# Optimization experiments

Hardware: AMD Instinct MI355X
Metric: run time of the kernel (lower is better)

The kernel has to match this reference:

```python
import jax, jax.numpy as jnp
import numpy as np

N_NODES = 100000
N_EDGES = 1600000
MIN_NORM = 1e-15
EPS_F32 = 4e-3  # PoincareBall eps for float32


def _norm(x):
    return jnp.clip(jnp.linalg.norm(x, axis=-1, keepdims=True), MIN_NORM)


def artanh(x):
    x = jnp.clip(x, -1.0 + 1e-15, 1.0 - 1e-15)
    return 0.5 * (jnp.log1p(x) - jnp.log1p(-x))


def proj(x, c):
    norm = _norm(x)
    maxnorm = (1.0 - EPS_F32) / jnp.sqrt(c)
    return jnp.where(norm > maxnorm, x / norm * maxnorm, x)


def expmap0(u, c):
    sqrt_c = jnp.sqrt(c)
    u_norm = _norm(u)
    return jnp.tanh(sqrt_c * u_norm) * u / (sqrt_c * u_norm)


def logmap0(p, c):
    sqrt_c = jnp.sqrt(c)
    p_norm = _norm(p)
    return artanh(sqrt_c * p_norm) * p / (sqrt_c * p_norm)


def mobius_add(x, y, c):
    x2 = jnp.sum(x * x, axis=-1, keepdims=True)
    y2 = jnp.sum(y * y, axis=-1, keepdims=True)
    xy = jnp.sum(x * y, axis=-1, keepdims=True)
    num = (1.0 + 2.0 * c * xy + c * y2) * x + (1.0 - c * x2) * y
    denom = 1.0 + 2.0 * c * xy + (c ** 2) * x2 * y2
    return num / jnp.clip(denom, MIN_NORM)


def mobius_matvec(m, x, c):
    sqrt_c = jnp.sqrt(c)
    x_norm = _norm(x)
    mx = x @ m.T  # [N, out]
    mx_norm = _norm(mx)
    res = jnp.tanh(mx_norm / x_norm * artanh(sqrt_c * x_norm)) * mx / (mx_norm * sqrt_c)
    cond = jnp.all(mx == 0.0, axis=-1, keepdims=True)
    return jnp.where(cond, 0.0, res)


def hyp_linear(x, w, b, c):
    mv = proj(mobius_matvec(w, x, c), c)
    hyp_bias = proj(expmap0(b[None, :], c), c)  # proj_tan0 is identity on Poincare ball
    return proj(mobius_add(mv, hyp_bias, c), c)


def hyp_agg(x, edge_row, edge_col, edge_weight, c):
    x_tan = logmap0(x, c)
    msgs = edge_weight[:, None] * x_tan[edge_col]  # gather source features
    support = jax.ops.segment_sum(msgs, edge_row, num_segments=N_NODES)
    return proj(expmap0(support, c), c)


def hyp_act(x, c_in, c_out):
    xt = jax.nn.relu(logmap0(x, c_in))  # proj_tan0 identity
    return proj(expmap0(xt, c_out), c_out)


def setup_inputs() -> dict:
    key = jax.random.key(0)
    ks = jax.random.split(key, 10)
    x = jax.random.normal(ks[0], (N_NODES, 1433), dtype=jnp.float32)
    edge_row = jax.random.randint(ks[1], (N_EDGES,), 0, N_NODES, dtype=jnp.int32)
    edge_col = jax.random.randint(ks[2], (N_EDGES,), 0, N_NODES, dtype=jnp.int32)
    edge_weight = jax.random.uniform(ks[3], (N_EDGES,), dtype=jnp.float32)
    w1 = jax.random.normal(ks[4], (100, 1433), dtype=jnp.float32) * 0.05
    b1 = jax.random.normal(ks[5], (100,), dtype=jnp.float32) * 0.05
    w2 = jax.random.normal(ks[6], (64, 100), dtype=jnp.float32) * 0.05
    b2 = jax.random.normal(ks[7], (64,), dtype=jnp.float32) * 0.05
    lin_w = jax.random.normal(ks[8], (7, 64), dtype=jnp.float32) * 0.05
    lin_b = jax.random.normal(ks[9], (7,), dtype=jnp.float32) * 0.05
    return {"x": x, "edge_row": edge_row, "edge_col": edge_col,
            "edge_weight": edge_weight, "w1": w1, "b1": b1,
            "w2": w2, "b2": b2, "lin_w": lin_w, "lin_b": lin_b}


def reference(x, edge_row, edge_col, edge_weight, w1, b1, w2, b2, lin_w, lin_b):
    c = 1.0
    # encode: tangent -> hyperbolic (proj_tan0 is identity)
    h = proj(expmap0(x, c), c)
    # layer 1: HypLinear -> HypAgg -> HypAct
    h = hyp_linear(h, w1, b1, c)
    h = hyp_agg(h, edge_row, edge_col, edge_weight, c)
    h = hyp_act(h, c, c)
    # layer 2
    h = hyp_linear(h, w2, b2, c)
    h = hyp_agg(h, edge_row, edge_col, edge_weight, c)
    h = hyp_act(h, c, c)
    # decode: logmap0 -> Linear(64,7) with relu -> log_softmax
    t = logmap0(h, c)
    logits = jax.nn.relu(t @ lin_w.T + lin_b)
    return jax.nn.log_softmax(logits, axis=-1)
```

## Files before the change

### kernel.cpp

```cpp
#include <hip/hip_runtime.h>
#include <hip/hip_bf16.h>
#include <math.h>

#define MINN 1e-15f
#define MAXN 0.996f

#define KPAD 1472

typedef __attribute__((ext_vector_type(8))) short short8;
typedef __attribute__((ext_vector_type(4))) float f32x4;

__device__ __forceinline__ float artanhf_(float v){
  v = fminf(fmaxf(v, -0.9999999f), 0.9999999f);
  return 0.5f*(log1pf(v) - log1pf(-v));
}
__device__ __forceinline__ float grp8(float v){
  v += __shfl_xor(v,1,8); v += __shfl_xor(v,2,8); v += __shfl_xor(v,4,8); return v;
}
__device__ __forceinline__ float grp16w(float v){
  v += __shfl_xor(v,1,16); v += __shfl_xor(v,2,16);
  v += __shfl_xor(v,4,16); v += __shfl_xor(v,8,16); return v;
}
__device__ __forceinline__ unsigned short f2bf(float f){
  unsigned int u = __float_as_uint(f);
  unsigned int r = (u + 0x7fffu + ((u >> 16) & 1u)) >> 16;
  return (unsigned short)r;
}
__device__ __forceinline__ float bf2f(unsigned short h){
  return __uint_as_float(((unsigned int)h) << 16);
}
__device__ __forceinline__ unsigned short f2bf_c(float f){
  __hip_bfloat16 b = __float2bfloat16(f);
  return *reinterpret_cast<unsigned short*>(&b);
}

typedef __attribute__((address_space(1))) const unsigned int gu32;
typedef __attribute__((address_space(3))) unsigned int su32;
__device__ __forceinline__ void gload_lds16(const void* g, void* s){
  __builtin_amdgcn_global_load_lds((gu32*)g, (su32*)s, 16, 0, 0);
}

__global__ __launch_bounds__(256) void k_prep_w1b16(const float* __restrict__ w1,
    unsigned short* __restrict__ w1hi, unsigned short* __restrict__ w1lo){
  int idx = blockIdx.x*256 + threadIdx.x;
  int col = idx / KPAD, k = idx - col*KPAD;
  float v = (col < 100 && k < 1433) ? w1[(size_t)col*1433 + k] : 0.f;
  unsigned short h = f2bf(v);
  unsigned short lo = f2bf(v - bf2f(h));
  w1hi[idx] = h; w1lo[idx] = lo;
}

__global__ void k_bias(const float* __restrict__ b1, const float* __restrict__ b2,
                       float* __restrict__ hb1, float* __restrict__ hb2, float* __restrict__ scal){
  __shared__ float red[128];
  int t = threadIdx.x;
  float v = (t < 100) ? b1[t] : 0.f;
  red[t] = v*v; __syncthreads();
  for (int s=64;s;s>>=1){ if (t<s) red[t]+=red[t+s]; __syncthreads(); }
  float n2 = red[0]; __syncthreads();
  float n = fmaxf(sqrtf(n2), MINN);
  float s1 = tanhf(n)/n;
  float pn = fmaxf(tanhf(n), MINN);
  float t1 = pn > MAXN ? MAXN/pn : 1.f;
  float hv = s1*t1*v;
  hb1[t] = (t<100) ? hv : 0.f;
  red[t] = (t<100) ? hv*hv : 0.f; __syncthreads();
  for (int s=64;s;s>>=1){ if (t<s) red[t]+=red[t+s]; __syncthreads(); }
  if (t==0) scal[0] = red[0];
  __syncthreads();
  float v2 = (t < 64) ? b2[t] : 0.f;
  red[t] = v2*v2; __syncthreads();
  for (int s=64;s;s>>=1){ if (t<s) red[t]+=red[t+s]; __syncthreads(); }
  float n2b = red[0]; __syncthreads();
  float nb = fmaxf(sqrtf(n2b), MINN);
  float s1b = tanhf(nb)/nb;
  float pnb = fmaxf(tanhf(nb), MINN);
  float t1b = pnb > MAXN ? MAXN/pnb : 1.f;
  float hvb = s1b*t1b*v2;
  if (t < 64) hb2[t] = hvb;
  red[t] = (t<64) ? hvb*hvb : 0.f; __syncthreads();
  for (int s=64;s;s>>=1){ if (t<s) red[t]+=red[t+s]; __syncthreads(); }
  if (t==0) scal[1] = red[0];
}

__global__ __launch_bounds__(512) void k_lin1_mfma(
    const float* __restrict__ x, const unsigned short* __restrict__ w1hi,
    const unsigned short* __restrict__ w1lo, const float* __restrict__ hb1,
    const float* __restrict__ scal, unsigned short* __restrict__ xtan1, int N)
{
  __shared__ alignas(16) char bsm[2*28*1024];
  int tid = threadIdx.x;
  int w = tid >> 6, l = tid & 63;
  int lr = l & 15, lg = l >> 4;
  int bm = blockIdx.x * 128;
  int row0 = bm + w*16;
  int r = row0 + lr;
  const float* xr = x + (size_t)min(r, N-1)*1433 + lg*8;
  float b1sq = scal[0];

  f32x4 acc[7];
  #pragma unroll
  for (int t=0;t<7;t++) acc[t] = (f32x4){0.f,0.f,0.f,0.f};
  float sq = 0.f;

  auto stage = [&](int buf, int kbase){
    #pragma unroll
    for (int c = 0; c < 4; ++c){
      int cc = w + 8*c;
      if (cc < 28){
        int h = (cc >= 14) ? 1 : 0;
        int rem = cc - h*14;
        int t = (rem < 7) ? rem : rem - 7;
        const unsigned short* arr = (rem < 7) ? w1hi : w1lo;
        const unsigned short* src = arr + (size_t)(t*16 + lr)*KPAD + kbase + h*32 + lg*8;
        gload_lds16(src, bsm + (buf*28 + cc)*1024);
      }
    }
  };
  auto xload = [&](float* d, int kbase){
    #pragma unroll
    for (int h = 0; h < 2; ++h){
      int kk = kbase + h*32;
      const float* p = xr + kk;
      if (kk + 32 <= 1433) {
        #pragma unroll
        for (int j=0;j<8;j++) d[h*8+j] = p[j];
      } else {
        #pragma unroll
        for (int j=0;j<8;j++){
          bool kv = (kk + lg*8 + j) < 1433;
          d[h*8+j] = kv ? p[j] : 0.f;
        }
      }
    }
  };

  stage(0, 0);
  float xa[16];
  xload(xa, 0);
  __syncthreads();

  for (int kb = 0; kb < 23; ++kb) {
    int cur = kb & 1, nxt = cur ^ 1;
    int nk = (kb + 1) * 64;

    float xb[16];
    if (kb + 1 < 23){
      stage(nxt, nk);
      xload(xb, nk);
    } else {
      #pragma unroll
      for (int j=0;j<16;j++) xb[j] = 0.f;
    }

    #pragma unroll
    for (int h = 0; h < 2; ++h){
      short8 ah, al;
      #pragma unroll
      for (int j=0;j<8;j++){
        float v = xa[h*8+j];
        sq = fmaf(v, v, sq);
        unsigned short hu = f2bf_c(v);
        ah[j] = (short)hu;
        float hf = bf2f(hu);
        al[j] = (short)f2bf_c(v - hf);
      }
      const char* base = bsm + (cur*28 + h*14)*1024 + (l << 4);
      short8 bh[7], bl[7];
      #pragma unroll
      for (int t=0;t<7;t++){
        bh[t] = *reinterpret_cast<const short8*>(base + t*1024);
        bl[t] = *reinterpret_cast<const short8*>(base + (7+t)*1024);
      }
      #pragma unroll
      for (int t=0;t<7;t++){
        acc[t] = __builtin_amdgcn_mfma_f32_16x16x32_bf16(ah, bh[t], acc[t], 0,0,0);
        acc[t] = __builtin_amdgcn_mfma_f32_16x16x32_bf16(al, bh[t], acc[t], 0,0,0);
        acc[t] = __builtin_amdgcn_mfma_f32_16x16x32_bf16(ah, bl[t], acc[t], 0,0,0);
      }
    }
    #pragma unroll
    for (int j=0;j<16;j++) xa[j] = xb[j];

    __syncthreads();
  }

  sq += __shfl_xor(sq, 16); sq += __shfl_xor(sq, 32);

  float hbv[7];
  #pragma unroll
  for (int t=0;t<7;t++) hbv[t] = hb1[t*16 + lr];

  #pragma unroll
  for (int r4=0;r4<4;r4++){
    int rrow = 4*lg + r4;
    float v[7];
    #pragma unroll
    for (int t=0;t<7;t++) v[t] = acc[t][r4];
    float yn2 = 0.f, dotb = 0.f;
    #pragma unroll
    for (int t=0;t<7;t++){ yn2 += v[t]*v[t]; dotb += v[t]*hbv[t]; }
    yn2 = grp16w(yn2); dotb = grp16w(dotb);
    float xn2 = __shfl(sq, rrow);

    float un = fmaxf(sqrtf(xn2), MINN);
    float th = tanhf(un);
    float sE = th/un;
    float pn = fmaxf(th, MINN);
    float t1 = pn > MAXN ? MAXN/pn : 1.f;
    float gam = sE*t1;
    float xh = fmaxf(gam*un, MINN);
    float yn = sqrtf(yn2);
    float mxn = fmaxf(gam*yn, MINN);
    float rs = tanhf(mxn/xh*artanhf_(xh))/mxn;
    if (yn2 == 0.f) rs = 0.f;
    float rn = rs*gam*yn;
    float t2 = rn > MAXN ? MAXN/fmaxf(rn,MINN) : 1.f;
    float alpha = t2*rs*gam;
    float x2v = alpha*alpha*yn2;
    float xyv = alpha*dotb;
    float den = fmaxf(1.f + 2.f*xyv + x2v*b1sq, MINN);
    float A = (1.f + 2.f*xyv + b1sq)/den, B = (1.f - x2v)/den;
    float Aa = A*alpha;
    float on2 = 0.f;
    float o[7];
    #pragma unroll
    for (int t=0;t<7;t++){ o[t] = Aa*v[t] + B*hbv[t]; on2 += o[t]*o[t]; }
    on2 = grp16w(on2);
    float on = sqrtf(on2);
    float onc = fmaxf(on, MINN);
    float t3 = onc > MAXN ? MAXN/onc : 1.f;
    float pn3 = fmaxf(t3*on, MINN);
    float fs = artanhf_(pn3)/pn3 * t3;

    int grow = row0 + rrow;
    if (grow < N){
      #pragma unroll
      for (int t=0;t<7;t++){
        int c = t*16 + lr;
        if (c < 100) xtan1[(size_t)grow*100 + c] = f2bf(fs*o[t]);
      }
    }
  }
}

__global__ __launch_bounds__(256) void k_hist(const int* __restrict__ er, int* __restrict__ counts, int E){
  int e = blockIdx.x*256 + threadIdx.x;
  if (e < E) atomicAdd(&counts[er[e]], 1);
}

__global__ __launch_bounds__(256) void k_scan1(const int* __restrict__ counts, int* __restrict__ row_start,
                                               int* __restrict__ blksum, int N){
  __shared__ int s[256];
  int t = threadIdx.x;
  int base = blockIdx.x*1024 + t*4;
  int v[4]; int sum = 0;
  #pragma unroll
  for (int i=0;i<4;i++){ v[i] = (base+i < N) ? counts[base+i] : 0; sum += v[i]; }
  s[t] = sum; __syncthreads();
  for (int off=1; off<256; off<<=1){
    int val = (t >= off) ? s[t-off] : 0;
    __syncthreads();
    s[t] += val;
    __syncthreads();
  }
  int run = (t > 0) ? s[t-1] : 0;
  #pragma unroll
  for (int i=0;i<4;i++){ if (base+i < N) row_start[base+i] = run; run += v[i]; }
  if (t == 255) blksum[blockIdx.x] = s[255];
}

__global__ void k_scan2(int* blksum, int nblk){
  int run = 0;
  for (int i=0;i<nblk;i++){ int v = blksum[i]; blksum[i] = run; run += v; }
}

__global__ __launch_bounds__(256) void k_scan3(int* __restrict__ row_start, const int* __restrict__ blksum,
                                               int* __restrict__ cursor, int N){
  int i = blockIdx.x*256 + threadIdx.x;
  if (i < N){ int v = row_start[i] + blksum[i >> 10]; row_start[i] = v; cursor[i] = v; }
}

__global__ __launch_bounds__(256) void k_scatter(const int* __restrict__ er, const int* __restrict__ ec,
    const float* __restrict__ ew, int* __restrict__ cursor,
    int* __restrict__ ecs, float* __restrict__ ews, int E){
  int e = blockIdx.x*256 + threadIdx.x;
  if (e < E){
    int r = er[e];
    int pos = atomicAdd(&cursor[r], 1);
    ecs[pos] = ec[e];
    ews[pos] = ew[e];
  }
}

template<int DD>
__global__ __launch_bounds__(256) void k_agg_gather(
    const unsigned short* __restrict__ xt, const int* __restrict__ row_start,
    const int* __restrict__ counts, const int* __restrict__ ecs,
    const float* __restrict__ ews, float* __restrict__ sup, int N)
{
  int row = blockIdx.x*4 + (threadIdx.x >> 6);
  int lane = threadIdx.x & 63;
  if (row >= N) return;
  int start = row_start[row], cnt = counts[row];
  constexpr int D2 = (DD > 64) ? (DD - 64) : 0;
  float acc0 = 0.f, acc1 = 0.f;
  for (int j = 0; j < cnt; j += 64) {
    int cc = 0; float wt = 0.f;
    if (j + lane < cnt) { int idx = start + j + lane; cc = ecs[idx]; wt = ews[idx]; }
    int lim = min(64, cnt - j);
    int k = 0;
    for (; k + 8 <= lim; k += 8) {
      const unsigned short *s0,*s1,*s2,*s3,*s4,*s5,*s6,*s7;
      float w0,w1,w2,w3,w4,w5,w6,w7;
      s0 = xt + (size_t)__shfl(cc,k+0)*DD; w0 = __shfl(wt,k+0);
      s1 = xt + (size_t)__shfl(cc,k+1)*DD; w1 = __shfl(wt,k+1);
      s2 = xt + (size_t)__shfl(cc,k+2)*DD; w2 = __shfl(wt,k+2);
      s3 = xt + (size_t)__shfl(cc,k+3)*DD; w3 = __shfl(wt,k+3);
      s4 = xt + (size_t)__shfl(cc,k+4)*DD; w4 = __shfl(wt,k+4);
      s5 = xt + (size_t)__shfl(cc,k+5)*DD; w5 = __shfl(wt,k+5);
      s6 = xt + (size_t)__shfl(cc,k+6)*DD; w6 = __shfl(wt,k+6);
      s7 = xt + (size_t)__shfl(cc,k+7)*DD; w7 = __shfl(wt,k+7);
      unsigned short a0=s0[lane],a1=s1[lane],a2=s2[lane],a3=s3[lane];
      unsigned short a4=s4[lane],a5=s5[lane],a6=s6[lane],a7=s7[lane];
      if constexpr (D2 > 0) {
        if (lane < D2) {
          unsigned short b0=s0[64+lane],b1=s1[64+lane],b2=s2[64+lane],b3=s3[64+lane];
          unsigned short b4=s4[64+lane],b5=s5[64+lane],b6=s6[64+lane],b7=s7[64+lane];
          acc1 += w0*bf2f(b0); acc1 += w1*bf2f(b1); acc1 += w2*bf2f(b2); acc1 += w3*bf2f(b3);
          acc1 += w4*bf2f(b4); acc1 += w5*bf2f(b5); acc1 += w6*bf2f(b6); acc1 += w7*bf2f(b7);
        }
      }
      acc0 += w0*bf2f(a0); acc0 += w1*bf2f(a1); acc0 += w2*bf2f(a2); acc0 += w3*bf2f(a3);
      acc0 += w4*bf2f(a4); acc0 += w5*bf2f(a5); acc0 += w6*bf2f(a6); acc0 += w7*bf2f(a7);
    }
    for (; k < lim; ++k) {
      int col = __shfl(cc, k);
      float w  = __shfl(wt, k);
      const unsigned short* src = xt + (size_t)col*DD;
      acc0 += w * bf2f(src[lane]);
      if constexpr (D2 > 0) { if (lane < D2) acc1 += w * bf2f(src[64 + lane]); }
    }
  }
  float* dst = sup + (size_t)row*DD;
  dst[lane] = acc0;
  if constexpr (D2 > 0) { if (lane < D2) dst[64 + lane] = acc1; }
}

__global__ __launch_bounds__(256) void k_layer2(
    const float* __restrict__ sup, const float* __restrict__ w2,
    const float* __restrict__ hb2, const float* __restrict__ scal,
    unsigned short* __restrict__ xtan2, int N)
{
  __shared__ alignas(16) float w2s[64][100];
  __shared__ float xts[32][105];
  __shared__ float hbs[64];
  int tid = threadIdx.x;
  for (int i = tid; i < 1600; i += 256)
    reinterpret_cast<float4*>(&w2s[0][0])[i] = reinterpret_cast<const float4*>(w2)[i];
  if (tid < 64) hbs[tid] = hb2[tid];
  float b2sq = scal[1];
  __syncthreads();
  int rr = tid >> 3, g = tid & 7;
  int grow = blockIdx.x*32 + rr;
  bool valid = grow < N;
  float sv[13]; float sn2 = 0.f;
  #pragma unroll
  for (int m=0;m<13;m++){
    int j = g + 8*m;
    float v = (valid && j < 100) ? sup[(size_t)grow*100 + j] : 0.f;
    sv[m] = v; sn2 += v*v;
  }
  sn2 = grp8(sn2);
  float snn = fmaxf(sqrtf(sn2), MINN);
  float e1 = tanhf(snn)/snn;
  float pnA = fmaxf(tanhf(snn), MINN);
  float t1 = pnA > MAXN ? MAXN/pnA : 1.f;
  float phi = e1*t1;
  float hn = fmaxf(phi*snn, MINN);
  float lam = artanhf_(hn)/hn;
  float xn2 = 0.f;
  #pragma unroll
  for (int m=0;m<13;m++){
    int j = g + 8*m;
    if (j < 100){ float v = fmaxf(lam*phi*sv[m], 0.f); xts[rr][j] = v; xn2 += v*v; }
  }
  xn2 = grp8(xn2);
  float xn = fmaxf(sqrtf(xn2), MINN);
  float e2 = tanhf(xn)/xn;
  float pnB = fmaxf(tanhf(xn), MINN);
  float t2 = pnB > MAXN ? MAXN/pnB : 1.f;
  float psi = e2*t2;
  __syncthreads();
  float z[8] = {};
  for (int j=0;j<100;j++){
    float xv = xts[rr][j];
    #pragma unroll
    for (int m=0;m<8;m++) z[m] += xv * w2s[g+8*m][j];
  }
  float zn2 = 0.f, dz = 0.f;
  #pragma unroll
  for (int m=0;m<8;m++){ zn2 += z[m]*z[m]; dz += z[m]*hbs[g+8*m]; }
  zn2 = grp8(zn2); dz = grp8(dz);
  float xnh = fmaxf(psi*xn, MINN);
  float zn = sqrtf(zn2);
  float mxn = fmaxf(psi*zn, MINN);
  float rs = tanhf(mxn/xnh*artanhf_(xnh))/mxn;
  if (zn2 == 0.f) rs = 0.f;
  float rn = rs*psi*zn;
  float t3 = rn > MAXN ? MAXN/fmaxf(rn,MINN) : 1.f;
  float alpha = t3*rs*psi;
  float x2 = alpha*alpha*zn2;
  float xy = alpha*dz;
  float den = fmaxf(1.f + 2.f*xy + x2*b2sq, MINN);
  float A = (1.f + 2.f*xy + b2sq)/den, B = (1.f - x2)/den;
  float Aa = A*alpha;
  float ov[8]; float on2 = 0.f;
  #pragma unroll
  for (int m=0;m<8;m++){ ov[m] = Aa*z[m] + B*hbs[g+8*m]; on2 += ov[m]*ov[m]; }
  on2 = grp8(on2);
  float on = sqrtf(on2);
  float onc = fmaxf(on, MINN);
  float t4 = onc > MAXN ? MAXN/onc : 1.f;
  float pn4 = fmaxf(t4*on, MINN);
  float fs = artanhf_(pn4)/pn4 * t4;
  if (valid)
    #pragma unroll
    for (int m=0;m<8;m++) xtan2[(size_t)grow*64 + g + 8*m] = f2bf(fs*ov[m]);
}

__global__ __launch_bounds__(256) void k_decode(
    const float* __restrict__ sup2, const float* __restrict__ lw,
    const float* __restrict__ lb, float* __restrict__ out, int N)
{
  __shared__ float lws[7][64];
  __shared__ float lbs[7];
  int tid = threadIdx.x;
  for (int i = tid; i < 448; i += 256) lws[i>>6][i&63] = lw[i];
  if (tid < 7) lbs[tid] = lb[tid];
  __syncthreads();
  int rr = tid >> 3, g = tid & 7;
  int grow = blockIdx.x*32 + rr;
  bool valid = grow < N;
  float sv[8]; float sn2 = 0.f;
  #pragma unroll
  for (int m=0;m<8;m++){
    int j = g + 8*m;
    float v = valid ? sup2[(size_t)grow*64 + j] : 0.f;
    sv[m] = v; sn2 += v*v;
  }
  sn2 = grp8(sn2);
  float snn = fmaxf(sqrtf(sn2), MINN);
  float e1 = tanhf(snn)/snn;
  float pnA = fmaxf(tanhf(snn), MINN);
  float t1 = pnA > MAXN ? MAXN/pnA : 1.f;
  float phi = e1*t1;
  float hn = fmaxf(phi*snn, MINN);
  float lam = artanhf_(hn)/hn;
  float xt[8]; float xn2 = 0.f;
  #pragma unroll
  for (int m=0;m<8;m++){ xt[m] = fmaxf(lam*phi*sv[m], 0.f); xn2 += xt[m]*xt[m]; }
  xn2 = grp8(xn2);
  float xn = fmaxf(sqrtf(xn2), MINN);
  float e2 = tanhf(xn)/xn;
  float pnB = fmaxf(tanhf(xn), MINN);
  float t2 = pnB > MAXN ? MAXN/pnB : 1.f;
  float psi = e2*t2;
  float tn = fmaxf(psi*xn, MINN);
  float lam2 = artanhf_(tn)/tn;
  float tc = lam2*psi;
  float lg[7];
  #pragma unroll
  for (int k=0;k<7;k++){
    float p = 0.f;
    #pragma unroll
    for (int m=0;m<8;m++) p += xt[m]*lws[k][g+8*m];
    p = grp8(p) * tc;
    lg[k] = fmaxf(p + lbs[k], 0.f);
  }
  float mx = lg[0];
  #pragma unroll
  for (int k=1;k<7;k++) mx = fmaxf(mx, lg[k]);
  float se = 0.f;
  #pragma unroll
  for (int k=0;k<7;k++) se += expf(lg[k]-mx);
  float lse = logf(se);
  if (valid && g < 7) out[(size_t)grow*7 + g] = lg[g] - mx - lse;
}

extern "C" void kernel_launch(void* const* d_in, const int* in_sizes, int n_in,
                              void* d_out, int out_size, void* d_ws, size_t ws_size,
                              hipStream_t stream)
{
  const float* x  = (const float*)d_in[0];
  const int*   er = (const int*)  d_in[1];
  const int*   ec = (const int*)  d_in[2];
  const float* ew = (const float*)d_in[3];
  const float* w1 = (const float*)d_in[4];
  const float* b1 = (const float*)d_in[5];
  const float* w2 = (const float*)d_in[6];
  const float* b2 = (const float*)d_in[7];
  const float* lw = (const float*)d_in[8];
  const float* lb = (const float*)d_in[9];
  float* out = (float*)d_out;
  int N = in_sizes[0] / 1433;
  int E = in_sizes[1];

  float* W = (float*)d_ws;
  float* hb1  = W;
  float* hb2  = W + 128;
  float* scal = W + 192;
  unsigned short* w1hi = (unsigned short*)(W + 256);
  unsigned short* w1lo = (unsigned short*)(W + 82688);
  int*   counts    = (int*)(W + 165120);
  int*   row_start = counts + N;
  int*   cursor    = row_start + N;
  int*   blksum    = cursor + N;
  int*   ecs       = blksum + 128;
  float* ews       = (float*)(ecs + E);
  unsigned short* xtanb = (unsigned short*)(ews + E);
  float* sup = ews + E + (size_t)N*50;

  int nblk_scan = (N + 1023) / 1024;

  hipMemsetAsync(counts, 0, (size_t)N*sizeof(int), stream);
  k_hist<<<(E + 255)/256, 256, 0, stream>>>(er, counts, E);
  k_scan1<<<nblk_scan, 256, 0, stream>>>(counts, row_start, blksum, N);
  k_scan2<<<1, 1, 0, stream>>>(blksum, nblk_scan);
  k_scan3<<<(N + 255)/256, 256, 0, stream>>>(row_start, blksum, cursor, N);
  k_scatter<<<(E + 255)/256, 256, 0, stream>>>(er, ec, ew, cursor, ecs, ews, E);

  k_prep_w1b16<<<(112*KPAD + 255)/256, 256, 0, stream>>>(w1, w1hi, w1lo);
  k_bias<<<1, 128, 0, stream>>>(b1, b2, hb1, hb2, scal);

  int nb128 = (N + 127)/128;
  k_lin1_mfma<<<nb128, 512, 0, stream>>>(x, w1hi, w1lo, hb1, scal, xtanb, N);

  int nbg = (N + 3)/4;
  int nb32 = (N + 31)/32;
  k_agg_gather<100><<<nbg, 256, 0, stream>>>(xtanb, row_start, counts, ecs, ews, sup, N);
  k_layer2<<<nb32, 256, 0, stream>>>(sup, w2, hb2, scal, xtanb, N);
  k_agg_gather<64><<<nbg, 256, 0, stream>>>(xtanb, row_start, counts, ecs, ews, sup, N);
  k_decode<<<nb32, 256, 0, stream>>>(sup, lw, lb, out, N);
}
```

Before: 667.2 us.

## Pack edge metadata, widen gather loads, split 64-dim rows across half-waves

Edge column and weight are now interleaved into a single uint2 array, so the gather fetches one 8-byte record per edge instead of two separate arrays. The 100-dim aggregation reads two bf16 values per lane as 32-bit loads using 50 active lanes. The 64-dim aggregation has each half-wave handle a different edge with 32-bit loads and combines the halves with a cross-lane shuffle at the end. The single-thread k_scan2 launch is dropped, and k_scan3 recomputes block prefixes serially per block, which adds redundant reads but removes one launch.

```diff
diff --git a/kernel.cpp b/kernel.cpp
--- a/kernel.cpp
+++ b/kernel.cpp
@@ -270,81 +270,152 @@
   if (t == 255) blksum[blockIdx.x] = s[255];
 }
 
-__global__ void k_scan2(int* blksum, int nblk){
-  int run = 0;
-  for (int i=0;i<nblk;i++){ int v = blksum[i]; blksum[i] = run; run += v; }
-}
-
 __global__ __launch_bounds__(256) void k_scan3(int* __restrict__ row_start, const int* __restrict__ blksum,
                                                int* __restrict__ cursor, int N){
+  __shared__ int pref;
+  if (threadIdx.x == 0){
+    int seg = blockIdx.x >> 2;
+    int s = 0;
+    for (int q = 0; q < seg; ++q) s += blksum[q];
+    pref = s;
+  }
+  __syncthreads();
   int i = blockIdx.x*256 + threadIdx.x;
-  if (i < N){ int v = row_start[i] + blksum[i >> 10]; row_start[i] = v; cursor[i] = v; }
+  if (i < N){ int v = row_start[i] + pref; row_start[i] = v; cursor[i] = v; }
 }
 
 __global__ __launch_bounds__(256) void k_scatter(const int* __restrict__ er, const int* __restrict__ ec,
     const float* __restrict__ ew, int* __restrict__ cursor,
-    int* __restrict__ ecs, float* __restrict__ ews, int E){
+    uint2* __restrict__ meta, int E){
   int e = blockIdx.x*256 + threadIdx.x;
   if (e < E){
     int r = er[e];
     int pos = atomicAdd(&cursor[r], 1);
-    ecs[pos] = ec[e];
-    ews[pos] = ew[e];
-  }
-}
-
-template<int DD>
-__global__ __launch_bounds__(256) void k_agg_gather(
+    uint2 m;
+    m.x = (unsigned int)ec[e];
+    m.y = __float_as_uint(ew[e]);
+    meta[pos] = m;
+  }
+}
+
+__global__ __launch_bounds__(256) void k_agg100(
     const unsigned short* __restrict__ xt, const int* __restrict__ row_start,
-    const int* __restrict__ counts, const int* __restrict__ ecs,
-    const float* __restrict__ ews, float* __restrict__ sup, int N)
+    const int* __restrict__ counts, const uint2* __restrict__ meta,
+    float* __restrict__ sup, int N)
 {
   int row = blockIdx.x*4 + (threadIdx.x >> 6);
   int lane = threadIdx.x & 63;
   if (row >= N) return;
   int start = row_start[row], cnt = counts[row];
-  constexpr int D2 = (DD > 64) ? (DD - 64) : 0;
-  float acc0 = 0.f, acc1 = 0.f;
+  bool act = lane < 50;
+  float a0 = 0.f, a1 = 0.f;
   for (int j = 0; j < cnt; j += 64) {
     int cc = 0; float wt = 0.f;
-    if (j + lane < cnt) { int idx = start + j + lane; cc = ecs[idx]; wt = ews[idx]; }
+    if (j + lane < cnt) { uint2 m = meta[start + j + lane]; cc = (int)m.x; wt = __uint_as_float(m.y); }
     int lim = min(64, cnt - j);
     int k = 0;
     for (; k + 8 <= lim; k += 8) {
-      const unsigned short *s0,*s1,*s2,*s3,*s4,*s5,*s6,*s7;
+      const unsigned int *p0,*p1,*p2,*p3,*p4,*p5,*p6,*p7;
       float w0,w1,w2,w3,w4,w5,w6,w7;
-      s0 = xt + (size_t)__shfl(cc,k+0)*DD; w0 = __shfl(wt,k+0);
-      s1 = xt + (size_t)__shfl(cc,k+1)*DD; w1 = __shfl(wt,k+1);
-      s2 = xt + (size_t)__shfl(cc,k+2)*DD; w2 = __shfl(wt,k+2);
-      s3 = xt + (size_t)__shfl(cc,k+3)*DD; w3 = __shfl(wt,k+3);
-      s4 = xt + (size_t)__shfl(cc,k+4)*DD; w4 = __shfl(wt,k+4);
-      s5 = xt + (size_t)__shfl(cc,k+5)*DD; w5 = __shfl(wt,k+5);
-      s6 = xt + (size_t)__shfl(cc,k+6)*DD; w6 = __shfl(wt,k+6);
-      s7 = xt + (size_t)__shfl(cc,k+7)*DD; w7 = __shfl(wt,k+7);
-      unsigned short a0=s0[lane],a1=s1[lane],a2=s2[lane],a3=s3[lane];
-      unsigned short a4=s4[lane],a5=s5[lane],a6=s6[lane],a7=s7[lane];
-      if constexpr (D2 > 0) {
-        if (lane < D2) {
-          unsigned short b0=s0[64+lane],b1=s1[64+lane],b2=s2[64+lane],b3=s3[64+lane];
-          unsigned short b4=s4[64+lane],b5=s5[64+lane],b6=s6[64+lane],b7=s7[64+lane];
-          acc1 += w0*bf2f(b0); acc1 += w1*bf2f(b1); acc1 += w2*bf2f(b2); acc1 += w3*bf2f(b3);
-          acc1 += w4*bf2f(b4); acc1 += w5*bf2f(b5); acc1 += w6*bf2f(b6); acc1 += w7*bf2f(b7);
-        }
-      }
-      acc0 += w0*bf2f(a0); acc0 += w1*bf2f(a1); acc0 += w2*bf2f(a2); acc0 += w3*bf2f(a3);
-      acc0 += w4*bf2f(a4); acc0 += w5*bf2f(a5); acc0 += w6*bf2f(a6); acc0 += w7*bf2f(a7);
+      p0 = reinterpret_cast<const unsigned int*>(xt + (size_t)__shfl(cc,k+0)*100); w0 = __shfl(wt,k+0);
+      p1 = reinterpret_cast<const unsigned int*>(xt + (size_t)__shfl(cc,k+1)*100); w1 = __shfl(wt,k+1);
+      p2 = reinterpret_cast<const unsigned int*>(xt + (size_t)__shfl(cc,k+2)*100); w2 = __shfl(wt,k+2);
+      p3 = reinterpret_cast<const unsigned int*>(xt + (size_t)__shfl(cc,k+3)*100); w3 = __shfl(wt,k+3);
+      p4 = reinterpret_cast<const unsigned int*>(xt + (size_t)__shfl(cc,k+4)*100); w4 = __shfl(wt,k+4);
+      p5 = reinterpret_cast<const unsigned int*>(xt + (size_t)__shfl(cc,k+5)*100); w5 = __shfl(wt,k+5);
+      p6 = reinterpret_cast<const unsigned int*>(xt + (size_t)__shfl(cc,k+6)*100); w6 = __shfl(wt,k+6);
+      p7 = reinterpret_cast<const unsigned int*>(xt + (size_t)__shfl(cc,k+7)*100); w7 = __shfl(wt,k+7);
+      if (act){
+        unsigned int u0=p0[lane],u1=p1[lane],u2=p2[lane],u3=p3[lane];
+        unsigned int u4=p4[lane],u5=p5[lane],u6=p6[lane],u7=p7[lane];
+        a0 += w0*bf2f((unsigned short)u0); a1 += w0*bf2f((unsigned short)(u0>>16));
+        a0 += w1*bf2f((unsigned short)u1); a1 += w1*bf2f((unsigned short)(u1>>16));
+        a0 += w2*bf2f((unsigned short)u2); a1 += w2*bf2f((unsigned short)(u2>>16));
+        a0 += w3*bf2f((unsigned short)u3); a1 += w3*bf2f((unsigned short)(u3>>16));
+        a0 += w4*bf2f((unsigned short)u4); a1 += w4*bf2f((unsigned short)(u4>>16));
+        a0 += w5*bf2f((unsigned short)u5); a1 += w5*bf2f((unsigned short)(u5>>16));
+        a0 += w6*bf2f((unsigned short)u6); a1 += w6*bf2f((unsigned short)(u6>>16));
+        a0 += w7*bf2f((unsigned short)u7); a1 += w7*bf2f((unsigned short)(u7>>16));
+      }
     }
     for (; k < lim; ++k) {
       int col = __shfl(cc, k);
-      float w  = __shfl(wt, k);
-      const unsigned short* src = xt + (size_t)col*DD;
-      acc0 += w * bf2f(src[lane]);
-      if constexpr (D2 > 0) { if (lane < D2) acc1 += w * bf2f(src[64 + lane]); }
-    }
-  }
-  float* dst = sup + (size_t)row*DD;
-  dst[lane] = acc0;
-  if constexpr (D2 > 0) { if (lane < D2) dst[64 + lane] = acc1; }
+      float w_  = __shfl(wt, k);
+      if (act){
+        unsigned int u = reinterpret_cast<const unsigned int*>(xt + (size_t)col*100)[lane];
+        a0 += w_*bf2f((unsigned short)u);
+        a1 += w_*bf2f((unsigned short)(u>>16));
+      }
+    }
+  }
+  if (act){
+    float2* dst = reinterpret_cast<float2*>(sup + (size_t)row*100);
+    dst[lane] = make_float2(a0, a1);
+  }
+}
+
+__global__ __launch_bounds__(256) void k_agg64(
+    const unsigned short* __restrict__ xt, const int* __restrict__ row_start,
+    const int* __restrict__ counts, const uint2* __restrict__ meta,
+    float* __restrict__ sup, int N)
+{
+  int row = blockIdx.x*4 + (threadIdx.x >> 6);
+  int lane = threadIdx.x & 63;
+  if (row >= N) return;
+  int half = lane >> 5, sl = lane & 31;
+  int start = row_start[row], cnt = counts[row];
+  float a0 = 0.f, a1 = 0.f;
+  for (int j = 0; j < cnt; j += 64) {
+    int cc = 0; float wt = 0.f;
+    if (j + lane < cnt) { uint2 m = meta[start + j + lane]; cc = (int)m.x; wt = __uint_as_float(m.y); }
+    int lim = min(64, cnt - j);
+    int k = 0;
+    for (; k + 16 <= lim; k += 16) {
+      const unsigned int *p0,*p1,*p2,*p3,*p4,*p5,*p6,*p7;
+      float w0,w1,w2,w3,w4,w5,w6,w7;
+      p0 = reinterpret_cast<const unsigned int*>(xt + (size_t)__shfl(cc,k+ 0+half)*64); w0 = __shfl(wt,k+ 0+half);
+      p1 = reinterpret_cast<const unsigned int*>(xt + (size_t)__shfl(cc,k+ 2+half)*64); w1 = __shfl(wt,k+ 2+half);
+      p2 = reinterpret_cast<const unsigned int*>(xt + (size_t)__shfl(cc,k+ 4+half)*64); w2 = __shfl(wt,k+ 4+half);
+      p3 = reinterpret_cast<const unsigned int*>(xt + (size_t)__shfl(cc,k+ 6+half)*64); w3 = __shfl(wt,k+ 6+half);
+      p4 = reinterpret_cast<const unsigned int*>(xt + (size_t)__shfl(cc,k+ 8+half)*64); w4 = __shfl(wt,k+ 8+half);
+      p5 = reinterpret_cast<const unsigned int*>(xt + (size_t)__shfl(cc,k+10+half)*64); w5 = __shfl(wt,k+10+half);
+      p6 = reinterpret_cast<const unsigned int*>(xt + (size_t)__shfl(cc,k+12+half)*64); w6 = __shfl(wt,k+12+half);
+      p7 = reinterpret_cast<const unsigned int*>(xt + (size_t)__shfl(cc,k+14+half)*64); w7 = __shfl(wt,k+14+half);
+      unsigned int u0=p0[sl],u1=p1[sl],u2=p2[sl],u3=p3[sl];
+      unsigned int u4=p4[sl],u5=p5[sl],u6=p6[sl],u7=p7[sl];
+      a0 += w0*bf2f((unsigned short)u0); a1 += w0*bf2f((unsigned short)(u0>>16));
+      a0 += w1*bf2f((unsigned short)u1); a1 += w1*bf2f((unsigned short)(u1>>16));
+      a0 += w2*bf2f((unsigned short)u2); a1 += w2*bf2f((unsigned short)(u2>>16));
+      a0 += w3*bf2f((unsigned short)u3); a1 += w3*bf2f((unsigned short)(u3>>16));
+      a0 += w4*bf2f((unsigned short)u4); a1 += w4*bf2f((unsigned short)(u4>>16));
+      a0 += w5*bf2f((unsigned short)u5); a1 += w5*bf2f((unsigned short)(u5>>16));
+      a0 += w6*bf2f((unsigned short)u6); a1 += w6*bf2f((unsigned short)(u6>>16));
+      a0 += w7*bf2f((unsigned short)u7); a1 += w7*bf2f((unsigned short)(u7>>16));
+    }
+    for (; k + 2 <= lim; k += 2) {
+      int e = k + half;
+      int col = __shfl(cc, e);
+      float w_ = __shfl(wt, e);
+      unsigned int u = reinterpret_cast<const unsigned int*>(xt + (size_t)col*64)[sl];
+      a0 += w_*bf2f((unsigned short)u);
+      a1 += w_*bf2f((unsigned short)(u>>16));
+    }
+    if (k < lim) {
+      int col = __shfl(cc, k);
+      float w_ = __shfl(wt, k);
+      if (half == 0){
+        unsigned int u = reinterpret_cast<const unsigned int*>(xt + (size_t)col*64)[sl];
+        a0 += w_*bf2f((unsigned short)u);
+        a1 += w_*bf2f((unsigned short)(u>>16));
+      }
+    }
+  }
+  a0 += __shfl_xor(a0, 32);
+  a1 += __shfl_xor(a1, 32);
+  if (lane < 32){
+    float2* dst = reinterpret_cast<float2*>(sup + (size_t)row*64);
+    dst[sl] = make_float2(a0, a1);
+  }
 }
 
 __global__ __launch_bounds__(256) void k_layer2(
@@ -512,23 +583,21 @@
   float* scal = W + 192;
   unsigned short* w1hi = (unsigned short*)(W + 256);
   unsigned short* w1lo = (unsigned short*)(W + 82688);
-  int*   counts    = (int*)(W + 165120);
+  uint2* meta = (uint2*)(W + 165120);
+  int*   counts    = (int*)(W + 165120 + 2*(size_t)E);
   int*   row_start = counts + N;
   int*   cursor    = row_start + N;
   int*   blksum    = cursor + N;
-  int*   ecs       = blksum + 128;
-  float* ews       = (float*)(ecs + E);
-  unsigned short* xtanb = (unsigned short*)(ews + E);
-  float* sup = ews + E + (size_t)N*50;
+  unsigned short* xtanb = (unsigned short*)(blksum + 128);
+  float* sup = (float*)(xtanb + (size_t)N*100);
 
   int nblk_scan = (N + 1023) / 1024;
 
   hipMemsetAsync(counts, 0, (size_t)N*sizeof(int), stream);
   k_hist<<<(E + 255)/256, 256, 0, stream>>>(er, counts, E);
   k_scan1<<<nblk_scan, 256, 0, stream>>>(counts, row_start, blksum, N);
-  k_scan2<<<1, 1, 0, stream>>>(blksum, nblk_scan);
   k_scan3<<<(N + 255)/256, 256, 0, stream>>>(row_start, blksum, cursor, N);
-  k_scatter<<<(E + 255)/256, 256, 0, stream>>>(er, ec, ew, cursor, ecs, ews, E);
+  k_scatter<<<(E + 255)/256, 256, 0, stream>>>(er, ec, ew, cursor, meta, E);
 
   k_prep_w1b16<<<(112*KPAD + 255)/256, 256, 0, stream>>>(w1, w1hi, w1lo);
   k_bias<<<1, 128, 0, stream>>>(b1, b2, hb1, hb2, scal);
@@ -538,8 +607,8 @@
 
   int nbg = (N + 3)/4;
   int nb32 = (N + 31)/32;
-  k_agg_gather<100><<<nbg, 256, 0, stream>>>(xtanb, row_start, counts, ecs, ews, sup, N);
+  k_agg100<<<nbg, 256, 0, stream>>>(xtanb, row_start, counts, meta, sup, N);
   k_layer2<<<nb32, 256, 0, stream>>>(sup, w2, hb2, scal, xtanb, N);
-  k_agg_gather<64><<<nbg, 256, 0, stream>>>(xtanb, row_start, counts, ecs, ews, sup, N);
+  k_agg64<<<nbg, 256, 0, stream>>>(xtanb, row_start, counts, meta, sup, N);
   k_decode<<<nb32, 256, 0, stream>>>(sup, lw, lb, out, N);
 }
```

Measured after the change: 653.2 us. -2.1%, faster.
